# Performance work log

Hardware: AMD Instinct MI355X
Metric: run time of the kernel (lower is better)

## Reference

```python
import jax, jax.numpy as jnp
import numpy as np

C = 1.0          # ball curvature
EPS = 1e-5


def _expmap0(x):
    rc = jnp.sqrt(C)
    n = jnp.maximum(jnp.linalg.norm(x, axis=-1, keepdims=True), EPS)
    return jnp.tanh(rc * n) * x / (rc * n)


def _logmap0(y):
    rc = jnp.sqrt(C)
    n = jnp.maximum(jnp.linalg.norm(y, axis=-1, keepdims=True), EPS)
    t = jnp.minimum(rc * n, 1.0 - EPS)  # keep artanh finite
    return jnp.arctanh(t) * y / (rc * n)


def _poincare_fc(x, z, bias):
    # Shimizu et al. (HNN++) Poincare fully-connected layer.
    rc = jnp.sqrt(C)
    z_norm = jnp.maximum(jnp.linalg.norm(z, axis=0), EPS)   # (out,)
    z_unit = z / z_norm                                     # (in, out)
    drcr = 2.0 * rc * bias                                  # (out,)
    rcx = rc * x                                            # (B, in)
    cx2 = jnp.minimum(jnp.sum(rcx * rcx, axis=-1, keepdims=True), 1.0 - EPS)  # (B,1)
    # unidirectional Poincare MLR per output unit
    num = (2.0 * (rcx @ z_unit)) * jnp.cosh(drcr) - (1.0 + cx2) * jnp.sinh(drcr)
    mlr = (2.0 * z_norm / rc) * jnp.arcsinh(num / (1.0 - cx2))  # (B, out)
    # lift back to the ball
    y = jnp.sinh(rc * mlr) / rc
    return y / (1.0 + jnp.sqrt(1.0 + C * jnp.sum(y * y, axis=-1, keepdims=True)))


def setup_inputs() -> dict:
    key = jax.random.key(0)
    k1, k2, k3 = jax.random.split(key, 3)
    B, DIN, DOUT = 8192, 4096, 4096
    x = jax.random.normal(k1, (B, DIN), dtype=jnp.float32) * 0.02  # small tangent vectors
    z = jax.random.normal(k2, (DIN, DOUT), dtype=jnp.float32) * (2.0 * DIN * DOUT) ** (-0.5)
    bias = jax.random.normal(k3, (DOUT,), dtype=jnp.float32) * 0.01
    return {"x": x, "z": z, "bias": bias}


def reference(x, z, bias):
    h = _expmap0(x)                 # tangent -> ball
    y = _poincare_fc(h, z, bias)    # Mobius/Poincare linear
    return _logmap0(y)              # ball -> tangent
```

## Files before the change

### kernel.cpp

```cpp
#include <hip/hip_runtime.h>
#include <hip/hip_bf16.h>
#include <math.h>

#define EPSF 1e-5f
#define LOG2E 1.4426950408889634f
#define LN2 0.6931471805599453f

typedef __attribute__((ext_vector_type(4))) float f32x4;
typedef __attribute__((ext_vector_type(8))) short s16x8;

__device__ __forceinline__ float hw_exp2(float x) { return __builtin_amdgcn_exp2f(x); }
__device__ __forceinline__ float hw_log2(float x) { return __builtin_amdgcn_logf(x); }
__device__ __forceinline__ float fast_rcp(float x) { return __builtin_amdgcn_rcpf(x); }

__device__ __forceinline__ float block_reduce_sum_256(float s) {
  #pragma unroll
  for (int o = 32; o > 0; o >>= 1) s += __shfl_xor(s, o, 64);
  __shared__ float red[4];
  int lane = threadIdx.x & 63, wid = threadIdx.x >> 6;
  if (lane == 0) red[wid] = s;
  __syncthreads();
  return red[0] + red[1] + red[2] + red[3];
}

__device__ __forceinline__ unsigned short f2bu(float f) {
  __hip_bfloat16 b = __float2bfloat16(f);
  return __builtin_bit_cast(unsigned short, b);
}

__global__ void k_expmap(const float* __restrict__ x, __hip_bfloat16* __restrict__ h,
                         float* __restrict__ cx2, float* __restrict__ invomc, int K) {
  int row = blockIdx.x, t = threadIdx.x;
  const float4* xr = (const float4*)(x + (size_t)row * K);
  float4 v[4];
  float s = 0.f;
  #pragma unroll
  for (int i = 0; i < 4; ++i) {
    v[i] = xr[t + (i << 8)];
    s += v[i].x * v[i].x + v[i].y * v[i].y + v[i].z * v[i].z + v[i].w * v[i].w;
  }
  float nsq = block_reduce_sum_256(s);
  float n = fmaxf(sqrtf(nsq), EPSF);
  float e2 = hw_exp2(2.f * LOG2E * n);
  float th = 1.f - 2.f * fast_rcp(e2 + 1.f);
  float sc = th * fast_rcp(n);
  float hn2 = sc * sc * nsq;
  float c2 = fminf(hn2, 1.f - EPSF);
  if (t == 0) { cx2[row] = c2; invomc[row] = 1.f / (1.f - c2); }
  ushort4* hr = (ushort4*)(h + (size_t)row * K);
  #pragma unroll
  for (int i = 0; i < 4; ++i) {
    ushort4 o;
    o.x = f2bu(sc * v[i].x); o.y = f2bu(sc * v[i].y);
    o.z = f2bu(sc * v[i].z); o.w = f2bu(sc * v[i].w);
    hr[t + (i << 8)] = o;
  }
}

__global__ void k_colsq(const float* __restrict__ z, float* __restrict__ part,
                        int K, int N, int rows_per_chunk) {
  int c4 = blockIdx.x * 256 + threadIdx.x;
  int r0 = blockIdx.y * rows_per_chunk;
  const float4* z4 = (const float4*)z;
  int n4 = N >> 2;
  float4 a = {0.f, 0.f, 0.f, 0.f};
  for (int r = r0; r < r0 + rows_per_chunk; ++r) {
    float4 v = z4[(size_t)r * n4 + c4];
    a.x += v.x * v.x; a.y += v.y * v.y; a.z += v.z * v.z; a.w += v.w * v.w;
  }
  ((float4*)part)[(size_t)blockIdx.y * n4 + c4] = a;
}

__global__ void k_colfin(const float* __restrict__ part, const float* __restrict__ bias,
                         float* __restrict__ zn2, float* __restrict__ invzn,
                         float* __restrict__ ch, float* __restrict__ sh,
                         int N, int nchunk) {
  int c = blockIdx.x * 256 + threadIdx.x;
  float s = 0.f;
  for (int i = 0; i < nchunk; ++i) s += part[(size_t)i * N + c];
  float zn = fmaxf(sqrtf(s), EPSF);
  zn2[c] = 2.f * zn;
  invzn[c] = 1.f / zn;
  float d = 2.f * bias[c];
  float ep = hw_exp2(LOG2E * d);
  float em = fast_rcp(ep);
  ch[c] = 0.5f * (ep + em);
  sh[c] = 0.5f * (ep - em);
}

__global__ void k_zunitT(const float* __restrict__ z, const float* __restrict__ invzn,
                         __hip_bfloat16* __restrict__ zt, int K, int N) {
  __shared__ float tile[32][33];
  int tx = threadIdx.x, ty = threadIdx.y;
  int c0 = blockIdx.x * 32, r0 = blockIdx.y * 32;
  float inv = invzn[c0 + tx];
  #pragma unroll
  for (int i = 0; i < 4; ++i)
    tile[ty + i * 8][tx] = z[(size_t)(r0 + ty + i * 8) * N + c0 + tx] * inv;
  __syncthreads();
  #pragma unroll
  for (int i = 0; i < 4; ++i)
    zt[(size_t)(c0 + ty + i * 8) * K + r0 + tx] = __float2bfloat16(tile[tx][ty + i * 8]);
}

template<int MQ, int NQ>
__device__ __forceinline__ void mm_phase(f32x4 (&acc)[8][4], const s16x8 (&av)[4][2],
                                         const s16x8 (&bv)[4][2]) {
  #pragma unroll
  for (int i = 0; i < 4; ++i) {
    #pragma unroll
    for (int jn = 0; jn < 2; ++jn) {
      acc[MQ * 4 + i][NQ * 2 + jn] = __builtin_amdgcn_mfma_f32_16x16x32_bf16(
          bv[NQ * 2 + jn][0], av[i][0], acc[MQ * 4 + i][NQ * 2 + jn], 0, 0, 0);
      acc[MQ * 4 + i][NQ * 2 + jn] = __builtin_amdgcn_mfma_f32_16x16x32_bf16(
          bv[NQ * 2 + jn][1], av[i][1], acc[MQ * 4 + i][NQ * 2 + jn], 0, 0, 0);
    }
  }
}

__device__ __forceinline__ const char* RFL64(const char* p) {
  unsigned long long b = (unsigned long long)p;
  unsigned int lo = __builtin_amdgcn_readfirstlane((unsigned int)b);
  unsigned int hi = __builtin_amdgcn_readfirstlane((unsigned int)(b >> 32));
  return (const char*)(((unsigned long long)hi << 32) | lo);
}

__global__ __launch_bounds__(512, 1) void k_gemm_dot(
    const __hip_bfloat16* __restrict__ A,
    const __hip_bfloat16* __restrict__ Bt,
    float* __restrict__ dot, int M, int N, int K) {
  __shared__ __align__(16) char smem[131072];
  const int K2 = K * 2;
  int tid = threadIdx.x, lane = tid & 63, wid = tid >> 6;
  int wm = wid >> 2, wn = wid & 3;

  int bid = blockIdx.x;
  int cpx = gridDim.x >> 3;
  int swz = (bid & 7) * cpx + (bid >> 3);
  int nbx = N >> 8;
  int bx = swz % nbx, by = swz / nbx;
  int bm0 = by * 256, bn0 = bx * 256;

  int rr = (tid >> 2) & 15;
  int cbyte = ((tid & 3) * 16) ^ ((rr & 8) << 2);
  int kb = ((tid >> 6) & 1) * 64 + cbyte;
  int r0 = ((tid >> 7) << 4) + rr;
  unsigned int off0 = (unsigned int)(r0 * K2 + kb);
  unsigned int off1 = off0 + (unsigned int)(64 * K2);
  int ldsW = wid * 1024;

  const char* aPan0 = (const char*)A + (size_t)bm0 * K2;
  const char* aPan1 = aPan0 + (size_t)128 * K2;
  const char* bPan0 = (const char*)Bt + (size_t)bn0 * K2;
  const char* bPan1 = bPan0 + (size_t)128 * K2;

  auto STAGE = [&](const char* base, int ldsBase) {
    __builtin_amdgcn_global_load_lds(
        (const __attribute__((address_space(1))) unsigned int*)(base + off0),
        (__attribute__((address_space(3))) unsigned int*)(smem + ldsBase + ldsW), 16, 0, 0);
    __builtin_amdgcn_global_load_lds(
        (const __attribute__((address_space(1))) unsigned int*)(base + off1),
        (__attribute__((address_space(3))) unsigned int*)(smem + ldsBase + ldsW + 8192), 16, 0, 0);
  };

  int labase = (lane & 15) * 64 + (((lane >> 4) * 16) ^ ((lane & 8) << 2));
  const char* pA0 = smem + wm * 16384 + labase;
  const char* pA1 = pA0 + 65536;
  const char* pB0 = smem + 32768 + (wn >> 1) * 16384 + (wn & 1) * 8192 + labase;
  const char* pB1 = pB0 + 65536;

  s16x8 av[4][2], bv[4][2];
  f32x4 acc[8][4] = {};

#define RDA(D, MQ) do { const char* p_ = ((D) ? pA1 : pA0); \
    _Pragma("unroll") for (int i_ = 0; i_ < 4; ++i_) { \
      av[i_][0] = *(const s16x8*)(p_ + (MQ) * 8192 + i_ * 2048); \
      av[i_][1] = *(const s16x8*)(p_ + (MQ) * 8192 + i_ * 2048 + 1024); } } while (0)
#define RDB01(D) do { const char* p_ = ((D) ? pB1 : pB0); \
    _Pragma("unroll") for (int f_ = 0; f_ < 2; ++f_) { \
      bv[f_][0] = *(const s16x8*)(p_ + f_ * 2048); \
      bv[f_][1] = *(const s16x8*)(p_ + f_ * 2048 + 1024); } } while (0)
#define RDB23(D) do { const char* p_ = ((D) ? pB1 : pB0); \
    _Pragma("unroll") for (int f_ = 2; f_ < 4; ++f_) { \
      bv[f_][0] = *(const s16x8*)(p_ + f_ * 2048); \
      bv[f_][1] = *(const s16x8*)(p_ + f_ * 2048 + 1024); } } while (0)

  int NT = K >> 6;

  {
    const char* a0 = RFL64(aPan0); const char* a1 = RFL64(aPan1);
    const char* b0 = RFL64(bPan0); const char* b1 = RFL64(bPan1);
    STAGE(b0, 32768); STAGE(b1, 49152); STAGE(a0, 0); STAGE(a1, 16384);
  }
  if (NT > 1) {
    const char* a0 = RFL64(aPan0 + 128); const char* a1 = RFL64(aPan1 + 128);
    const char* b0 = RFL64(bPan0 + 128); const char* b1 = RFL64(bPan1 + 128);
    STAGE(b0, 65536 + 32768); STAGE(b1, 65536 + 49152);
    STAGE(a0, 65536); STAGE(a1, 65536 + 16384);
    asm volatile("s_waitcnt vmcnt(8)");
  } else {
    asm volatile("s_waitcnt vmcnt(0)");
  }
  __builtin_amdgcn_s_barrier();

#define KTILE(D, KT) do { \
    bool pf_ = ((KT) + 2 < NT); \
    int kOff2_ = ((KT) + 2) << 7; \
    const char* aB0_ = RFL64(aPan0 + kOff2_); \
    const char* aB1_ = RFL64(aPan1 + kOff2_); \
    const char* bB0_ = RFL64(bPan0 + kOff2_); \
    const char* bB1_ = RFL64(bPan1 + kOff2_); \
     \
    RDA(D, 0); RDB01(D); \
    __builtin_amdgcn_s_barrier(); \
    asm volatile("s_waitcnt lgkmcnt(0)"); \
    __builtin_amdgcn_s_setprio(1); mm_phase<0, 0>(acc, av, bv); __builtin_amdgcn_s_setprio(0); \
    __builtin_amdgcn_s_barrier(); \
     \
    RDB23(D); \
    __builtin_amdgcn_s_barrier(); \
    asm volatile("s_waitcnt lgkmcnt(0)"); \
    __builtin_amdgcn_s_setprio(1); mm_phase<0, 1>(acc, av, bv); __builtin_amdgcn_s_setprio(0); \
    __builtin_amdgcn_s_barrier(); \
     \
    RDA(D, 1); \
    if (pf_) { STAGE(bB0_, (D) * 65536 + 32768); STAGE(bB1_, (D) * 65536 + 49152); } \
    __builtin_amdgcn_s_barrier(); \
    asm volatile("s_waitcnt lgkmcnt(0)"); \
    __builtin_amdgcn_s_setprio(1); mm_phase<1, 0>(acc, av, bv); __builtin_amdgcn_s_setprio(0); \
    __builtin_amdgcn_s_barrier(); \
     \
    if (pf_) { STAGE(aB0_, (D) * 65536); STAGE(aB1_, (D) * 65536 + 16384); } \
    __builtin_amdgcn_s_barrier(); \
    __builtin_amdgcn_s_setprio(1); mm_phase<1, 1>(acc, av, bv); __builtin_amdgcn_s_setprio(0); \
    if (pf_) { asm volatile("s_waitcnt vmcnt(8)"); } \
    else     { asm volatile("s_waitcnt vmcnt(0)"); } \
    __builtin_amdgcn_s_barrier(); \
  } while (0)

  for (int kt = 0; kt < NT; kt += 2) {
    KTILE(0, kt);
    KTILE(1, kt + 1);
  }
#undef KTILE
#undef RDA
#undef RDB01
#undef RDB23

  int ml = lane & 15, ng = lane >> 4;
  #pragma unroll
  for (int fm = 0; fm < 8; ++fm) {
    int row = bm0 + wm * 128 + fm * 16 + ml;
    size_t rowo = (size_t)row * N + bn0 + wn * 64 + ng * 4;
    #pragma unroll
    for (int fn = 0; fn < 4; ++fn) {
      *(f32x4*)(dot + rowo + fn * 16) = acc[fm][fn];
    }
  }
}

__global__ void k_mlr_final(float* __restrict__ io, const float* __restrict__ cx2,
                            const float* __restrict__ invomc, const float* __restrict__ zn2,
                            const float* __restrict__ chb, const float* __restrict__ shb,
                            int N) {
  int row = blockIdx.x, t = threadIdx.x;
  float4* ior = (float4*)(io + (size_t)row * N);
  const float4* ch4 = (const float4*)chb;
  const float4* sh4 = (const float4*)shb;
  const float4* z24 = (const float4*)zn2;
  float c2 = cx2[row], inv = invomc[row];
  float opc = 1.f + c2;
  float y[4][4];
  float s = 0.f;
  #pragma unroll
  for (int i = 0; i < 4; ++i) {
    int idx = t + (i << 8);
    float4 d = ior[idx], ch = ch4[idx], sh = sh4[idx], z2 = z24[idx];
    float dq[4] = {d.x, d.y, d.z, d.w};
    float chq[4] = {ch.x, ch.y, ch.z, ch.w};
    float shq[4] = {sh.x, sh.y, sh.z, sh.w};
    float zq[4] = {z2.x, z2.y, z2.z, z2.w};
    #pragma unroll
    for (int q = 0; q < 4; ++q) {
      float u = (2.f * dq[q] * chq[q] - opc * shq[q]) * inv;
      float w = u + sqrtf(fmaf(u, u, 1.f));
      float p = hw_log2(w);
      float tq = zq[q] * p;
      float ep = hw_exp2(tq);
      float em = hw_exp2(-tq);
      float yy = 0.5f * (ep - em);
      y[i][q] = yy;
      s += yy * yy;
    }
  }
  float ny2 = block_reduce_sum_256(s);
  float ny = sqrtf(ny2);
  float sfac = fast_rcp(1.f + sqrtf(1.f + ny2));
  float w = sfac * ny;
  float nw = fmaxf(w, EPSF);
  float tt = fminf(nw, 1.f - EPSF);
  float la = 0.5f * LN2 * hw_log2((1.f + tt) * fast_rcp(1.f - tt));
  float coef = la * sfac * fast_rcp(nw);
  #pragma unroll
  for (int i = 0; i < 4; ++i) {
    int idx = t + (i << 8);
    float4 o;
    o.x = coef * y[i][0]; o.y = coef * y[i][1];
    o.z = coef * y[i][2]; o.w = coef * y[i][3];
    ior[idx] = o;
  }
}

extern "C" void kernel_launch(void* const* d_in, const int* in_sizes, int n_in,
                              void* d_out, int out_size, void* d_ws, size_t ws_size,
                              hipStream_t stream) {
  const float* x    = (const float*)d_in[0];
  const float* z    = (const float*)d_in[1];
  const float* bias = (const float*)d_in[2];
  float* out = (float*)d_out;

  int N = in_sizes[2];
  int K = in_sizes[1] / N;
  int M = in_sizes[0] / K;

  char* ws = (char*)d_ws;
  size_t o = 0;
  __hip_bfloat16* h  = (__hip_bfloat16*)(ws + o); o += (size_t)M * K * 2;
  __hip_bfloat16* zt = (__hip_bfloat16*)(ws + o); o += (size_t)N * K * 2;
  float* cx2    = (float*)(ws + o); o += (size_t)M * 4;
  float* invomc = (float*)(ws + o); o += (size_t)M * 4;
  float* part   = (float*)(ws + o); o += (size_t)32 * N * 4;
  float* zn2    = (float*)(ws + o); o += (size_t)N * 4;
  float* invzn  = (float*)(ws + o); o += (size_t)N * 4;
  float* chb    = (float*)(ws + o); o += (size_t)N * 4;
  float* shb    = (float*)(ws + o); o += (size_t)N * 4;

  const int NCH = 32;
  k_expmap<<<M, 256, 0, stream>>>(x, h, cx2, invomc, K);
  k_colsq<<<dim3(N / 1024, NCH), 256, 0, stream>>>(z, part, K, N, K / NCH);
  k_colfin<<<N / 256, 256, 0, stream>>>(part, bias, zn2, invzn, chb, shb, N, NCH);
  k_zunitT<<<dim3(N / 32, K / 32), dim3(32, 8), 0, stream>>>(z, invzn, zt, K, N);
  int grid = (M / 256) * (N / 256);
  k_gemm_dot<<<grid, 512, 0, stream>>>(h, zt, out, M, N, K);
  k_mlr_final<<<M, 256, 0, stream>>>(out, cx2, invomc, zn2, chb, shb, N);
}
```

Measured before the change: 417.8 us.

## Split A fragments into two register sets and cut barriers in GEMM k-tile

The GEMM inner k-tile now keeps both halves of the A fragments in separate register arrays (av0/av1). The second half is read earlier, together with the B23 fragments, so the third phase needs no LDS reads of its own. This allows several s_barrier calls per k-tile to be removed, and all four prefetch stages are issued together before the last MFMA phase. The extra fragment registers raise VGPR pressure and could lower occupancy or cause spills. The reordered stage issue also changes how global-to-LDS loads overlap with compute.

```diff
diff --git a/kernel.cpp b/kernel.cpp
--- a/kernel.cpp
+++ b/kernel.cpp
@@ -169,13 +169,17 @@
   const char* pB0 = smem + 32768 + (wn >> 1) * 16384 + (wn & 1) * 8192 + labase;
   const char* pB1 = pB0 + 65536;
 
-  s16x8 av[4][2], bv[4][2];
+  s16x8 av0[4][2], av1[4][2], bv[4][2];
   f32x4 acc[8][4] = {};
 
-#define RDA(D, MQ) do { const char* p_ = ((D) ? pA1 : pA0); \
+#define RDA0(D) do { const char* p_ = ((D) ? pA1 : pA0); \
     _Pragma("unroll") for (int i_ = 0; i_ < 4; ++i_) { \
-      av[i_][0] = *(const s16x8*)(p_ + (MQ) * 8192 + i_ * 2048); \
-      av[i_][1] = *(const s16x8*)(p_ + (MQ) * 8192 + i_ * 2048 + 1024); } } while (0)
+      av0[i_][0] = *(const s16x8*)(p_ + i_ * 2048); \
+      av0[i_][1] = *(const s16x8*)(p_ + i_ * 2048 + 1024); } } while (0)
+#define RDA1(D) do { const char* p_ = ((D) ? pA1 : pA0); \
+    _Pragma("unroll") for (int i_ = 0; i_ < 4; ++i_) { \
+      av1[i_][0] = *(const s16x8*)(p_ + 8192 + i_ * 2048); \
+      av1[i_][1] = *(const s16x8*)(p_ + 8192 + i_ * 2048 + 1024); } } while (0)
 #define RDB01(D) do { const char* p_ = ((D) ? pB1 : pB0); \
     _Pragma("unroll") for (int f_ = 0; f_ < 2; ++f_) { \
       bv[f_][0] = *(const s16x8*)(p_ + f_ * 2048); \
@@ -211,28 +215,22 @@
     const char* bB0_ = RFL64(bPan0 + kOff2_); \
     const char* bB1_ = RFL64(bPan1 + kOff2_); \
      \
-    RDA(D, 0); RDB01(D); \
-    __builtin_amdgcn_s_barrier(); \
+    RDA0(D); RDB01(D); \
     asm volatile("s_waitcnt lgkmcnt(0)"); \
-    __builtin_amdgcn_s_setprio(1); mm_phase<0, 0>(acc, av, bv); __builtin_amdgcn_s_setprio(0); \
+    __builtin_amdgcn_s_setprio(1); mm_phase<0, 0>(acc, av0, bv); __builtin_amdgcn_s_setprio(0); \
     __builtin_amdgcn_s_barrier(); \
      \
-    RDB23(D); \
-    __builtin_amdgcn_s_barrier(); \
+    RDA1(D); RDB23(D); \
     asm volatile("s_waitcnt lgkmcnt(0)"); \
-    __builtin_amdgcn_s_setprio(1); mm_phase<0, 1>(acc, av, bv); __builtin_amdgcn_s_setprio(0); \
+    __builtin_amdgcn_s_setprio(1); mm_phase<0, 1>(acc, av0, bv); __builtin_amdgcn_s_setprio(0); \
     __builtin_amdgcn_s_barrier(); \
      \
-    RDA(D, 1); \
-    if (pf_) { STAGE(bB0_, (D) * 65536 + 32768); STAGE(bB1_, (D) * 65536 + 49152); } \
-    __builtin_amdgcn_s_barrier(); \
-    asm volatile("s_waitcnt lgkmcnt(0)"); \
-    __builtin_amdgcn_s_setprio(1); mm_phase<1, 0>(acc, av, bv); __builtin_amdgcn_s_setprio(0); \
+    __builtin_amdgcn_s_setprio(1); mm_phase<1, 0>(acc, av1, bv); __builtin_amdgcn_s_setprio(0); \
     __builtin_amdgcn_s_barrier(); \
      \
-    if (pf_) { STAGE(aB0_, (D) * 65536); STAGE(aB1_, (D) * 65536 + 16384); } \
-    __builtin_amdgcn_s_barrier(); \
-    __builtin_amdgcn_s_setprio(1); mm_phase<1, 1>(acc, av, bv); __builtin_amdgcn_s_setprio(0); \
+    if (pf_) { STAGE(bB0_, (D) * 65536 + 32768); STAGE(bB1_, (D) * 65536 + 49152); \
+               STAGE(aB0_, (D) * 65536); STAGE(aB1_, (D) * 65536 + 16384); } \
+    __builtin_amdgcn_s_setprio(1); mm_phase<1, 1>(acc, av1, bv); __builtin_amdgcn_s_setprio(0); \
     if (pf_) { asm volatile("s_waitcnt vmcnt(8)"); } \
     else     { asm volatile("s_waitcnt vmcnt(0)"); } \
     __builtin_amdgcn_s_barrier(); \
@@ -243,7 +241,8 @@
     KTILE(1, kt + 1);
   }
 #undef KTILE
-#undef RDA
+#undef RDA0
+#undef RDA1
 #undef RDB01
 #undef RDB23
 
```

Result: no change. 422.8 us (+1.2%).
